# Kernel tuning notes

Measured on AMD Instinct MI355X. Metric: run time of the kernel, lower is better.

Reference implementation:

```python
import jax, jax.numpy as jnp
import numpy as np

B, S, N_USERS, N_ITEMS, E = 32, 512, 10000, 10000, 128


def setup_inputs() -> dict:
    key = jax.random.key(0)
    ks = jax.random.split(key, 8)
    users = jax.random.randint(ks[0], (B, S), 0, N_USERS, dtype=jnp.int32)
    items = jax.random.randint(ks[1], (B, S), 0, N_ITEMS, dtype=jnp.int32)
    user_mem0 = jax.random.normal(ks[2], (B, N_USERS, E), dtype=jnp.float32)
    item_mem0 = jax.random.normal(ks[3], (B, N_ITEMS, E), dtype=jnp.float32)
    # GRUCell(2E, E): w_ih (3E, 2E), w_hh (3E, E)
    w_ih = jax.random.normal(ks[4], (3 * E, 2 * E), dtype=jnp.float32) * 0.05
    w_hh = jax.random.normal(ks[5], (3 * E, E), dtype=jnp.float32) * 0.05
    b_ih = jax.random.normal(ks[6], (3 * E,), dtype=jnp.float32) * 0.05
    b_hh = jax.random.normal(ks[7], (3 * E,), dtype=jnp.float32) * 0.05
    return {"users": users, "items": items, "user_mem0": user_mem0,
            "item_mem0": item_mem0, "w_ih": w_ih, "w_hh": w_hh,
            "b_ih": b_ih, "b_hh": b_hh}


def _gru_cell(x, h, w_ih, w_hh, b_ih, b_hh):
    # torch.nn.GRUCell semantics
    gi = x @ w_ih.T + b_ih  # (B, 3E)
    gh = h @ w_hh.T + b_hh  # (B, 3E)
    i_r, i_z, i_n = jnp.split(gi, 3, axis=-1)
    h_r, h_z, h_n = jnp.split(gh, 3, axis=-1)
    r = jax.nn.sigmoid(i_r + h_r)
    z = jax.nn.sigmoid(i_z + h_z)
    n = jnp.tanh(i_n + r * h_n)
    return (1.0 - z) * n + z * h


def reference(users, items, user_mem0, item_mem0, w_ih, w_hh, b_ih, b_hh):
    batch = jnp.arange(users.shape[0])

    def step(carry, uv):
        um, im = carry
        u, it = uv  # (B,), (B,)
        ue = um[batch, u]   # gather (B, E)
        ie = im[batch, it]  # gather (B, E)
        xu = jnp.concatenate([ue, ie], axis=-1)
        xi = jnp.concatenate([ie, ue], axis=-1)
        nu = _gru_cell(xu, ue, w_ih, w_hh, b_ih, b_hh)
        ni = _gru_cell(xi, ie, w_ih, w_hh, b_ih, b_hh)
        um = um.at[batch, u].set(nu)   # scatter write
        im = im.at[batch, it].set(ni)  # scatter write
        return (um, im), (nu, ni)

    (_, _), (u_out, i_out) = jax.lax.scan(
        step, (user_mem0, item_mem0), (users.T, items.T))
    # (S, B, E) -> (B, S, E)
    return jnp.transpose(u_out, (1, 0, 2)), jnp.transpose(i_out, (1, 0, 2))
```

## Files before the change

### kernel.cpp

```cpp
#include <hip/hip_runtime.h>

#define NB 32
#define NS 512
#define NE 128
#define NU 10000

#define WS_PREVU 0
#define WS_PREVI 16384
#define WS_RCNT  32768
#define WS_LCNT  32864
#define WS_GL    32896
#define WS_LATE  82048
#define WS_WBF   98432

typedef __attribute__((ext_vector_type(8))) short bf16x8;
typedef __attribute__((ext_vector_type(4))) float f32x4;

__device__ __forceinline__ unsigned short f2bf(float f) {
    unsigned int u = __float_as_uint(f);
    u += 0x7fff + ((u >> 16) & 1);
    return (unsigned short)(u >> 16);
}

__global__ __launch_bounds__(512) void prep_kernel(
    const int* __restrict__ users, const int* __restrict__ items,
    const float* __restrict__ w_ih, const float* __restrict__ w_hh, int* ws)
{
    const int blk = blockIdx.x, tid = threadIdx.x;
    if (blk >= 32) {
        const int base = (blk - 32) * 4096 + tid * 8;
        const int r = base >> 7, k = base & 127;
        const float* src;
        if (r < 384)      src = w_ih + (size_t)r * 256 + k;
        else if (r < 768) src = w_ih + (size_t)(r - 384) * 256 + 128 + k;
        else              src = w_hh + (size_t)(r - 768) * 128 + k;
        unsigned short* wbf = (unsigned short*)(ws + WS_WBF);
#pragma unroll
        for (int j = 0; j < 8; ++j) wbf[base + j] = f2bf(src[j]);
        return;
    }
    const int b = blk;
    __shared__ int s_u[NS], s_i[NS];
    __shared__ unsigned char s_r[NS];
    __shared__ int cnt[3], s_chg;
    s_u[tid] = users[b * NS + tid];
    s_i[tid] = items[b * NS + tid];
    if (tid < 3) cnt[tid] = 0;
    __syncthreads();
    const int mu = s_u[tid], mi = s_i[tid];
    int pu = -1, pi = -1;
    for (int u = tid - 1; u >= 0 && pu < 0; u -= 8) {
        int vals[8];
#pragma unroll
        for (int j = 0; j < 8; ++j) {
            const int uu = u - j;
            vals[j] = (uu >= 0) ? s_u[uu] : -1;
        }
#pragma unroll
        for (int j = 0; j < 8; ++j)
            if (pu < 0 && vals[j] == mu) pu = u - j;
    }
    for (int u = tid - 1; u >= 0 && pi < 0; u -= 8) {
        int vals[8];
#pragma unroll
        for (int j = 0; j < 8; ++j) {
            const int uu = u - j;
            vals[j] = (uu >= 0) ? s_i[uu] : -1;
        }
#pragma unroll
        for (int j = 0; j < 8; ++j)
            if (pi < 0 && vals[j] == mi) pi = u - j;
    }
    ws[WS_PREVU + (b << 9) + tid] = pu;
    ws[WS_PREVI + (b << 9) + tid] = pi;
    s_r[tid] = (pu < 0 && pi < 0) ? 0 : 255;
    __syncthreads();
    for (int pass = 0; pass < 16; ++pass) {
        if (tid == 0) s_chg = 0;
        __syncthreads();
        if (s_r[tid] == 255) {
            const int ru = pu < 0 ? -1 : (int)s_r[pu];
            const int ri = pi < 0 ? -1 : (int)s_r[pi];
            if (ru != 255 && ri != 255) {
                int rr = 1 + (ru > ri ? ru : ri);
                if (rr > 3) rr = 3;
                s_r[tid] = (unsigned char)rr;
                s_chg = 1;
            }
        }
        __syncthreads();
        if (!s_chg) break;
    }
    const int r = s_r[tid];
    if (r < 3) {
        const int slot = atomicAdd(&cnt[r], 1);
        ws[WS_GL + (r * 32 + b) * 512 + slot] = tid;
    }
    __syncthreads();
    if (tid < 3) ws[WS_RCNT + tid * 32 + b] = cnt[tid];
    if (tid == 0) {
        int n = 0;
        for (int t = 0; t < NS; ++t)
            if (s_r[t] >= 3) { ws[WS_LATE + (b << 9) + n] = t; ++n; }
        ws[WS_LCNT + b] = n;
    }
}

__global__ __launch_bounds__(512, 1) void rg0_kernel(
    const int* __restrict__ users, const int* __restrict__ items,
    const float* __restrict__ umem0, const float* __restrict__ imem0,
    const float* __restrict__ b_ih, const float* __restrict__ b_hh,
    const int* __restrict__ ws, float* uout, float* iout)
{
    const int b = blockIdx.x & 31, sblk = blockIdx.x >> 5;
    const int cnt = ws[WS_RCNT + b];
    const int nch = (cnt + 7) >> 3;
    if (sblk >= nch) return;
    const int tid = threadIdx.x;
    const int lane = tid & 63, wave = tid >> 6;
    const int col = lane & 15, kgrp = lane >> 4;

    __shared__ __align__(16) float yl[16 * 1156];
    __shared__ __align__(16) float xf[16 * 132];
    __shared__ __align__(16) unsigned short xb[16 * 136];
    __shared__ float b6[768];
    __shared__ unsigned long long srcs[16];
    __shared__ unsigned long long hdst[16];

    for (int i = tid; i < 768; i += 512)
        b6[i] = i < 384 ? b_ih[i] : b_hh[i - 384];

    const unsigned short* wbf = (const unsigned short*)(ws + WS_WBF);
    bf16x8 wfrag[9][4];
#pragma unroll
    for (int m9 = 0; m9 < 9; ++m9) {
        const int row = wave * 144 + m9 * 16 + col;
#pragma unroll
        for (int kt = 0; kt < 4; ++kt)
            wfrag[m9][kt] = *(const bf16x8*)&wbf[row * 128 + kt * 32 + kgrp * 8];
    }

    const int* glist = ws + WS_GL + b * 512;

    for (int lc = sblk; lc < nch; lc += 8) {
        if (tid < 16) {
            const int j = lc * 8 + (tid >> 1);
            unsigned long long sp = 0, hd = 0;
            if (j < cnt) {
                const int t = glist[j];
                const int node = (b << 9) + t;
                const int cell = tid & 1;
                const int ix = cell ? items[node] : users[node];
                sp = (unsigned long long)((cell ? imem0 : umem0)
                                          + ((size_t)b * NU + ix) * NE);
                hd = (unsigned long long)((cell ? iout : uout) + (size_t)node * NE);
            }
            srcs[tid] = sp; hdst[tid] = hd;
        }
        __syncthreads();
        {
            const int c = tid >> 5, e4 = (tid & 31) * 4;
            const float* s = (const float*)srcs[c];
            if (s) {
                const float4 vv = *(const float4*)(s + e4);
                *(float4*)&xf[c * 132 + e4] = vv;
                ushort4 w4;
                w4.x = f2bf(vv.x); w4.y = f2bf(vv.y);
                w4.z = f2bf(vv.z); w4.w = f2bf(vv.w);
                *(ushort4*)&xb[c * 136 + e4] = w4;
            }
        }
        __syncthreads();
        {
            bf16x8 bfrag[4];
#pragma unroll
            for (int kt = 0; kt < 4; ++kt)
                bfrag[kt] = *(const bf16x8*)&xb[col * 136 + kt * 32 + kgrp * 8];
            f32x4 acc[9];
#pragma unroll
            for (int m9 = 0; m9 < 9; ++m9) acc[m9] = (f32x4){0.f, 0.f, 0.f, 0.f};
#pragma unroll
            for (int kt = 0; kt < 4; ++kt)
#pragma unroll
                for (int m9 = 0; m9 < 9; ++m9)
                    acc[m9] = __builtin_amdgcn_mfma_f32_16x16x32_bf16(
                        wfrag[m9][kt], bfrag[kt], acc[m9], 0, 0, 0);
#pragma unroll
            for (int m9 = 0; m9 < 9; ++m9)
                *(f32x4*)&yl[col * 1156 + wave * 144 + m9 * 16 + kgrp * 4] = acc[m9];
        }
        __syncthreads();
#pragma unroll
        for (int it = 0; it < 4; ++it) {
            const int idx = tid + it * 512;
            const int c = idx >> 7, e = idx & 127;
            float* hb = (float*)hdst[c];
            if (hb) {
                const float* ys = &yl[c * 1156];
                const float* yo = &yl[(c ^ 1) * 1156];
                const float gir = ys[e]        + yo[384 + e] + b6[e];
                const float giz = ys[128 + e]  + yo[512 + e] + b6[128 + e];
                const float gin = ys[256 + e]  + yo[640 + e] + b6[256 + e];
                const float ghr = ys[768 + e]  + b6[384 + e];
                const float ghz = ys[896 + e]  + b6[512 + e];
                const float ghn = ys[1024 + e] + b6[640 + e];
                const float rr = 1.f / (1.f + __expf(-(gir + ghr)));
                const float z  = 1.f / (1.f + __expf(-(giz + ghz)));
                const float pre = gin + rr * ghn;
                const float nn = 2.f / (1.f + __expf(-2.f * pre)) - 1.f;
                hb[e] = (1.f - z) * nn + z * xf[c * 132 + e];
            }
        }
        __syncthreads();
    }
}

__global__ __launch_bounds__(512, 1) void finish_kernel(
    const int* __restrict__ users, const int* __restrict__ items,
    const float* __restrict__ umem0, const float* __restrict__ imem0,
    const float* __restrict__ b_ih, const float* __restrict__ b_hh,
    const int* __restrict__ ws, float* uout, float* iout)
{
    const int b = blockIdx.x;
    const int tid = threadIdx.x;
    const int lane = tid & 63, wave = tid >> 6;
    const int col = lane & 15, kgrp = lane >> 4;

    const int cnt1 = ws[WS_RCNT + 32 + b];
    const int cnt2 = ws[WS_RCNT + 64 + b];
    const int cntL = ws[WS_LCNT + b];
    if (cnt1 + cnt2 + cntL == 0) return;

    __shared__ __align__(16) float yl[16 * 1156];
    __shared__ __align__(16) float xf[16 * 132];
    __shared__ __align__(16) unsigned short xb[16 * 136];
    __shared__ float b6[768];
    __shared__ unsigned long long srcs[16];
    __shared__ unsigned long long hdst[16];

    for (int i = tid; i < 768; i += 512)
        b6[i] = i < 384 ? b_ih[i] : b_hh[i - 384];

    const unsigned short* wbf = (const unsigned short*)(ws + WS_WBF);
    bf16x8 wfrag[9][4];
#pragma unroll
    for (int m9 = 0; m9 < 9; ++m9) {
        const int row = wave * 144 + m9 * 16 + col;
#pragma unroll
        for (int kt = 0; kt < 4; ++kt)
            wfrag[m9][kt] = *(const bf16x8*)&wbf[row * 128 + kt * 32 + kgrp * 8];
    }

    const int* prevU = ws + WS_PREVU + (b << 9);
    const int* prevI = ws + WS_PREVI + (b << 9);

    for (int ph = 0; ph < 3; ++ph) {
        int base, cntn, step;
        if (ph == 0)      { cntn = cnt1; base = WS_GL + (32 + b) * 512;  step = 8; }
        else if (ph == 1) { cntn = cnt2; base = WS_GL + (64 + b) * 512;  step = 8; }
        else              { cntn = cntL; base = WS_LATE + (b << 9);      step = 1; }
        for (int j0 = 0; j0 < cntn; j0 += step) {
            const int n = (cntn - j0 < step) ? (cntn - j0) : step;
            if (tid < 16) {
                const int jj = tid >> 1;
                unsigned long long sp = 0, hd = 0;
                if (jj < n) {
                    const int t = ws[base + j0 + jj];
                    const int node = (b << 9) + t;
                    const int cell = tid & 1;
                    const int p = cell ? prevI[t] : prevU[t];
                    const float* s;
                    if (p < 0) {
                        const int ix = cell ? items[node] : users[node];
                        s = (cell ? imem0 : umem0) + ((size_t)b * NU + ix) * NE;
                    } else {
                        s = (cell ? iout : uout) + ((size_t)((b << 9) + p)) * NE;
                    }
                    sp = (unsigned long long)s;
                    hd = (unsigned long long)((cell ? iout : uout) + (size_t)node * NE);
                }
                srcs[tid] = sp; hdst[tid] = hd;
            }
            __syncthreads();
            {
                const int c = tid >> 5, e4 = (tid & 31) * 4;
                const float* s = (const float*)srcs[c];
                if (s) {
                    const float4 vv = *(const float4*)(s + e4);
                    *(float4*)&xf[c * 132 + e4] = vv;
                    ushort4 w4;
                    w4.x = f2bf(vv.x); w4.y = f2bf(vv.y);
                    w4.z = f2bf(vv.z); w4.w = f2bf(vv.w);
                    *(ushort4*)&xb[c * 136 + e4] = w4;
                }
            }
            __syncthreads();
            {
                bf16x8 bfrag[4];
#pragma unroll
                for (int kt = 0; kt < 4; ++kt)
                    bfrag[kt] = *(const bf16x8*)&xb[col * 136 + kt * 32 + kgrp * 8];
                f32x4 acc[9];
#pragma unroll
                for (int m9 = 0; m9 < 9; ++m9) acc[m9] = (f32x4){0.f, 0.f, 0.f, 0.f};
#pragma unroll
                for (int kt = 0; kt < 4; ++kt)
#pragma unroll
                    for (int m9 = 0; m9 < 9; ++m9)
                        acc[m9] = __builtin_amdgcn_mfma_f32_16x16x32_bf16(
                            wfrag[m9][kt], bfrag[kt], acc[m9], 0, 0, 0);
#pragma unroll
                for (int m9 = 0; m9 < 9; ++m9)
                    *(f32x4*)&yl[col * 1156 + wave * 144 + m9 * 16 + kgrp * 4] = acc[m9];
            }
            __syncthreads();
#pragma unroll
            for (int it = 0; it < 4; ++it) {
                const int idx = tid + it * 512;
                const int c = idx >> 7, e = idx & 127;
                float* hb = (float*)hdst[c];
                if (hb) {
                    const float* ys = &yl[c * 1156];
                    const float* yo = &yl[(c ^ 1) * 1156];
                    const float gir = ys[e]        + yo[384 + e] + b6[e];
                    const float giz = ys[128 + e]  + yo[512 + e] + b6[128 + e];
                    const float gin = ys[256 + e]  + yo[640 + e] + b6[256 + e];
                    const float ghr = ys[768 + e]  + b6[384 + e];
                    const float ghz = ys[896 + e]  + b6[512 + e];
                    const float ghn = ys[1024 + e] + b6[640 + e];
                    const float rr = 1.f / (1.f + __expf(-(gir + ghr)));
                    const float z  = 1.f / (1.f + __expf(-(giz + ghz)));
                    const float pre = gin + rr * ghn;
                    const float nn = 2.f / (1.f + __expf(-2.f * pre)) - 1.f;
                    hb[e] = (1.f - z) * nn + z * xf[c * 132 + e];
                }
            }
            __threadfence();
            __syncthreads();
        }
    }
}

extern "C" void kernel_launch(void* const* d_in, const int* in_sizes, int n_in,
                              void* d_out, int out_size, void* d_ws, size_t ws_size,
                              hipStream_t stream) {
    const int*   users = (const int*)d_in[0];
    const int*   items = (const int*)d_in[1];
    const float* umem0 = (const float*)d_in[2];
    const float* imem0 = (const float*)d_in[3];
    const float* w_ih  = (const float*)d_in[4];
    const float* w_hh  = (const float*)d_in[5];
    const float* b_ih  = (const float*)d_in[6];
    const float* b_hh  = (const float*)d_in[7];

    float* uout = (float*)d_out;
    float* iout = uout + (size_t)NB * NS * NE;
    int* ws = (int*)d_ws;

    prep_kernel<<<68, 512, 0, stream>>>(users, items, w_ih, w_hh, ws);
    rg0_kernel<<<256, 512, 0, stream>>>(users, items, umem0, imem0,
                                        b_ih, b_hh, ws, uout, iout);
    finish_kernel<<<NB, 512, 0, stream>>>(users, items, umem0, imem0,
                                          b_ih, b_hh, ws, uout, iout);
}
```

Before: 148.0 us.

## Run dependency rank 1 as parallel grid kernel and prefetch next chunk's gathers

Generalizes the rank-0 grid kernel to any rank and launches it a second time for rank 1, so those steps run across 256 blocks instead of 32 serial blocks in the finish kernel. The cleanup kernel now handles only rank 2 and the late list. Inside the grid kernel, chunk metadata and the gathered source row are software-prefetched one iteration ahead with double-buffered shared arrays, and __syncthreads is replaced by a lighter lgkmcnt-wait barrier. The prep kernel merges the two predecessor searches into one loop. This adds one more kernel launch, and the custom barrier relies on no outstanding global stores needing visibility across the barrier.

```diff
diff --git a/kernel.cpp b/kernel.cpp
--- a/kernel.cpp
+++ b/kernel.cpp
@@ -21,6 +21,12 @@
     u += 0x7fff + ((u >> 16) & 1);
     return (unsigned short)(u >> 16);
 }
+
+#define BARRIER() do { \
+    asm volatile("s_waitcnt lgkmcnt(0)" ::: "memory"); \
+    __builtin_amdgcn_s_barrier(); \
+    __builtin_amdgcn_sched_barrier(0); \
+} while (0)
 
 __global__ __launch_bounds__(512) void prep_kernel(
     const int* __restrict__ users, const int* __restrict__ items,
@@ -49,27 +55,19 @@
     __syncthreads();
     const int mu = s_u[tid], mi = s_i[tid];
     int pu = -1, pi = -1;
-    for (int u = tid - 1; u >= 0 && pu < 0; u -= 8) {
-        int vals[8];
+    for (int u = tid - 1; u >= 0 && ((pu < 0) | (pi < 0)); u -= 8) {
+        int vu[8], vi[8];
 #pragma unroll
         for (int j = 0; j < 8; ++j) {
             const int uu = u - j;
-            vals[j] = (uu >= 0) ? s_u[uu] : -1;
-        }
-#pragma unroll
-        for (int j = 0; j < 8; ++j)
-            if (pu < 0 && vals[j] == mu) pu = u - j;
-    }
-    for (int u = tid - 1; u >= 0 && pi < 0; u -= 8) {
-        int vals[8];
+            vu[j] = (uu >= 0) ? s_u[uu] : -1;
+            vi[j] = (uu >= 0) ? s_i[uu] : -1;
+        }
 #pragma unroll
         for (int j = 0; j < 8; ++j) {
-            const int uu = u - j;
-            vals[j] = (uu >= 0) ? s_i[uu] : -1;
-        }
-#pragma unroll
-        for (int j = 0; j < 8; ++j)
-            if (pi < 0 && vals[j] == mi) pi = u - j;
+            if (pu < 0 && vu[j] == mu) pu = u - j;
+            if (pi < 0 && vi[j] == mi) pi = u - j;
+        }
     }
     ws[WS_PREVU + (b << 9) + tid] = pu;
     ws[WS_PREVI + (b << 9) + tid] = pi;
@@ -106,14 +104,14 @@
     }
 }
 
-__global__ __launch_bounds__(512, 1) void rg0_kernel(
+__global__ __launch_bounds__(512, 1) void rg_kernel(
     const int* __restrict__ users, const int* __restrict__ items,
     const float* __restrict__ umem0, const float* __restrict__ imem0,
     const float* __restrict__ b_ih, const float* __restrict__ b_hh,
-    const int* __restrict__ ws, float* uout, float* iout)
+    const int* __restrict__ ws, float* uout, float* iout, int r)
 {
     const int b = blockIdx.x & 31, sblk = blockIdx.x >> 5;
-    const int cnt = ws[WS_RCNT + b];
+    const int cnt = ws[WS_RCNT + r * 32 + b];
     const int nch = (cnt + 7) >> 3;
     if (sblk >= nch) return;
     const int tid = threadIdx.x;
@@ -124,8 +122,8 @@
     __shared__ __align__(16) float xf[16 * 132];
     __shared__ __align__(16) unsigned short xb[16 * 136];
     __shared__ float b6[768];
-    __shared__ unsigned long long srcs[16];
-    __shared__ unsigned long long hdst[16];
+    __shared__ unsigned long long srcs[2][16];
+    __shared__ unsigned long long hdst[2][16];
 
     for (int i = tid; i < 768; i += 512)
         b6[i] = i < 384 ? b_ih[i] : b_hh[i - 384];
@@ -140,37 +138,60 @@
             wfrag[m9][kt] = *(const bf16x8*)&wbf[row * 128 + kt * 32 + kgrp * 8];
     }
 
-    const int* glist = ws + WS_GL + b * 512;
+    const int* glist = ws + WS_GL + (r * 32 + b) * 512;
+    const int* prevU = ws + WS_PREVU + (b << 9);
+    const int* prevI = ws + WS_PREVI + (b << 9);
+
+#define META(LC, SEL) do { \
+    if (tid < 16) { \
+        const int j = (LC) * 8 + (tid >> 1); \
+        unsigned long long sp = 0, hd = 0; \
+        if (j < cnt) { \
+            const int t = glist[j]; \
+            const int node = (b << 9) + t; \
+            const int cell = tid & 1; \
+            const int p = cell ? prevI[t] : prevU[t]; \
+            const float* s; \
+            if (p < 0) { \
+                const int ix = cell ? items[node] : users[node]; \
+                s = (cell ? imem0 : umem0) + ((size_t)b * NU + ix) * NE; \
+            } else { \
+                s = (cell ? iout : uout) + ((size_t)((b << 9) + p)) * NE; \
+            } \
+            sp = (unsigned long long)s; \
+            hd = (unsigned long long)((cell ? iout : uout) + (size_t)node * NE); \
+        } \
+        srcs[SEL][tid] = sp; hdst[SEL][tid] = hd; \
+    } \
+} while (0)
+
+    const int gc = tid >> 5, ge4 = (tid & 31) * 4;
+    int cur = 0;
+    META(sblk, 0);
+    BARRIER();
+    float4 v = (float4){0.f, 0.f, 0.f, 0.f};
+    {
+        const float* s = (const float*)srcs[0][gc];
+        if (s) v = *(const float4*)(s + ge4);
+    }
 
     for (int lc = sblk; lc < nch; lc += 8) {
-        if (tid < 16) {
-            const int j = lc * 8 + (tid >> 1);
-            unsigned long long sp = 0, hd = 0;
-            if (j < cnt) {
-                const int t = glist[j];
-                const int node = (b << 9) + t;
-                const int cell = tid & 1;
-                const int ix = cell ? items[node] : users[node];
-                sp = (unsigned long long)((cell ? imem0 : umem0)
-                                          + ((size_t)b * NU + ix) * NE);
-                hd = (unsigned long long)((cell ? iout : uout) + (size_t)node * NE);
-            }
-            srcs[tid] = sp; hdst[tid] = hd;
-        }
-        __syncthreads();
-        {
-            const int c = tid >> 5, e4 = (tid & 31) * 4;
-            const float* s = (const float*)srcs[c];
-            if (s) {
-                const float4 vv = *(const float4*)(s + e4);
-                *(float4*)&xf[c * 132 + e4] = vv;
-                ushort4 w4;
-                w4.x = f2bf(vv.x); w4.y = f2bf(vv.y);
-                w4.z = f2bf(vv.z); w4.w = f2bf(vv.w);
-                *(ushort4*)&xb[c * 136 + e4] = w4;
-            }
-        }
-        __syncthreads();
+        const int nxt = cur ^ 1;
+        const bool hasnext = (lc + 8) < nch;
+        if (hasnext) META(lc + 8, nxt);
+        if (hdst[cur][gc]) {
+            *(float4*)&xf[gc * 132 + ge4] = v;
+            ushort4 w4;
+            w4.x = f2bf(v.x); w4.y = f2bf(v.y);
+            w4.z = f2bf(v.z); w4.w = f2bf(v.w);
+            *(ushort4*)&xb[gc * 136 + ge4] = w4;
+        }
+        BARRIER();
+        float4 vn = (float4){0.f, 0.f, 0.f, 0.f};
+        if (hasnext) {
+            const float* s = (const float*)srcs[nxt][gc];
+            if (s) vn = *(const float4*)(s + ge4);
+        }
         {
             bf16x8 bfrag[4];
 #pragma unroll
@@ -189,12 +210,12 @@
             for (int m9 = 0; m9 < 9; ++m9)
                 *(f32x4*)&yl[col * 1156 + wave * 144 + m9 * 16 + kgrp * 4] = acc[m9];
         }
-        __syncthreads();
+        BARRIER();
 #pragma unroll
         for (int it = 0; it < 4; ++it) {
             const int idx = tid + it * 512;
             const int c = idx >> 7, e = idx & 127;
-            float* hb = (float*)hdst[c];
+            float* hb = (float*)hdst[cur][c];
             if (hb) {
                 const float* ys = &yl[c * 1156];
                 const float* yo = &yl[(c ^ 1) * 1156];
@@ -211,25 +232,25 @@
                 hb[e] = (1.f - z) * nn + z * xf[c * 132 + e];
             }
         }
-        __syncthreads();
-    }
-}
-
-__global__ __launch_bounds__(512, 1) void finish_kernel(
+        BARRIER();
+        v = vn; cur = nxt;
+    }
+#undef META
+}
+
+__global__ __launch_bounds__(512, 1) void cleanup_kernel(
     const int* __restrict__ users, const int* __restrict__ items,
     const float* __restrict__ umem0, const float* __restrict__ imem0,
     const float* __restrict__ b_ih, const float* __restrict__ b_hh,
     const int* __restrict__ ws, float* uout, float* iout)
 {
     const int b = blockIdx.x;
+    const int cnt2 = ws[WS_RCNT + 64 + b];
+    const int cntL = ws[WS_LCNT + b];
+    if (cnt2 + cntL == 0) return;
     const int tid = threadIdx.x;
     const int lane = tid & 63, wave = tid >> 6;
     const int col = lane & 15, kgrp = lane >> 4;
-
-    const int cnt1 = ws[WS_RCNT + 32 + b];
-    const int cnt2 = ws[WS_RCNT + 64 + b];
-    const int cntL = ws[WS_LCNT + b];
-    if (cnt1 + cnt2 + cntL == 0) return;
 
     __shared__ __align__(16) float yl[16 * 1156];
     __shared__ __align__(16) float xf[16 * 132];
@@ -254,11 +275,10 @@
     const int* prevU = ws + WS_PREVU + (b << 9);
     const int* prevI = ws + WS_PREVI + (b << 9);
 
-    for (int ph = 0; ph < 3; ++ph) {
-        int base, cntn, step;
-        if (ph == 0)      { cntn = cnt1; base = WS_GL + (32 + b) * 512;  step = 8; }
-        else if (ph == 1) { cntn = cnt2; base = WS_GL + (64 + b) * 512;  step = 8; }
-        else              { cntn = cntL; base = WS_LATE + (b << 9);      step = 1; }
+    for (int ph = 0; ph < 2; ++ph) {
+        const int cntn = ph == 0 ? cnt2 : cntL;
+        const int base = ph == 0 ? WS_GL + (64 + b) * 512 : WS_LATE + (b << 9);
+        const int step = ph == 0 ? 8 : 1;
         for (int j0 = 0; j0 < cntn; j0 += step) {
             const int n = (cntn - j0 < step) ? (cntn - j0) : step;
             if (tid < 16) {
@@ -358,8 +378,10 @@
     int* ws = (int*)d_ws;
 
     prep_kernel<<<68, 512, 0, stream>>>(users, items, w_ih, w_hh, ws);
-    rg0_kernel<<<256, 512, 0, stream>>>(users, items, umem0, imem0,
-                                        b_ih, b_hh, ws, uout, iout);
-    finish_kernel<<<NB, 512, 0, stream>>>(users, items, umem0, imem0,
-                                          b_ih, b_hh, ws, uout, iout);
-}
+    rg_kernel<<<256, 512, 0, stream>>>(users, items, umem0, imem0,
+                                       b_ih, b_hh, ws, uout, iout, 0);
+    rg_kernel<<<256, 512, 0, stream>>>(users, items, umem0, imem0,
+                                       b_ih, b_hh, ws, uout, iout, 1);
+    cleanup_kernel<<<NB, 512, 0, stream>>>(users, items, umem0, imem0,
+                                           b_ih, b_hh, ws, uout, iout);
+}
```

New measurement: 125.7 us. 15.1% less time.
